# Kernel tuning notes

Measured on AMD Instinct MI355X. Metric: run time of the kernel, lower is better.

## Reference

```python
import jax, jax.numpy as jnp
import numpy as np

B, C, H, W = 64, 2048, 14, 14
D, S, ITERS, EPS, HID = 256, 8, 3, 1e-8, 512


def build_pos(h, w, d):
    gy, gx = np.meshgrid(np.arange(h), np.arange(w), indexing='ij')
    q = d // 4
    omega = 1.0 / (10000.0 ** (np.arange(q) / q))
    ey = gy.reshape(-1, 1) * omega
    ex = gx.reshape(-1, 1) * omega
    pe = np.concatenate([np.sin(ey), np.cos(ey), np.sin(ex), np.cos(ex)], axis=1)
    return jnp.asarray(pe[None], jnp.float32)  # (1, h*w, d)


def layernorm(x, g, b, eps=1e-5):
    m = x.mean(-1, keepdims=True)
    v = ((x - m) ** 2).mean(-1, keepdims=True)
    return (x - m) * jax.lax.rsqrt(v + eps) * g + b


def setup_inputs() -> dict:
    key = jax.random.key(0)
    ks = jax.random.split(key, 16)
    w = lambda k, shp, s=0.02: jax.random.normal(k, shp, jnp.float32) * s
    inp = {
        'x': jax.random.normal(ks[0], (B, C, H, W), jnp.float32),
        'slot_noise': jax.random.normal(ks[1], (B, S, D), jnp.float32),
        'conv_w': w(ks[2], (C, D)), 'conv_b': jnp.zeros((D,), jnp.float32),
        'pos': build_pos(H, W, D),
        'slots_mu': jax.random.normal(ks[3], (1, 1, D), jnp.float32),
        'slots_logsigma': -jnp.ones((1, 1, D), jnp.float32),
        'qw': w(ks[4], (D, D)), 'qb': jnp.zeros((D,), jnp.float32),
        'kw': w(ks[5], (D, D)), 'kb': jnp.zeros((D,), jnp.float32),
        'vw': w(ks[6], (D, D)), 'vb': jnp.zeros((D,), jnp.float32),
        'gru_wih': w(ks[7], (D, 3 * D)), 'gru_whh': w(ks[8], (D, 3 * D)),
        'gru_bih': jnp.zeros((3 * D,), jnp.float32), 'gru_bhh': jnp.zeros((3 * D,), jnp.float32),
        'w1': w(ks[9], (D, HID)), 'b1': jnp.zeros((HID,), jnp.float32),
        'w2': w(ks[10], (HID, D)), 'b2': jnp.zeros((D,), jnp.float32),
        'ln_in_g': jnp.ones((D,), jnp.float32), 'ln_in_b': jnp.zeros((D,), jnp.float32),
        'ln_s_g': jnp.ones((D,), jnp.float32), 'ln_s_b': jnp.zeros((D,), jnp.float32),
        'ln_ff_g': jnp.ones((D,), jnp.float32), 'ln_ff_b': jnp.zeros((D,), jnp.float32),
    }
    return inp


def reference(x, slot_noise, conv_w, conv_b, pos, slots_mu, slots_logsigma,
              qw, qb, kw, kb, vw, vb, gru_wih, gru_whh, gru_bih, gru_bhh,
              w1, b1, w2, b2, ln_in_g, ln_in_b, ln_s_g, ln_s_b, ln_ff_g, ln_ff_b):
    b, c, h, w_ = x.shape
    d = qw.shape[0]
    scale = d ** (-0.5)
    # (B,C,H,W) -> (B,N,C) -> project -> add pos
    xt = x.transpose(0, 2, 3, 1).reshape(b, h * w_, c)
    xt = xt @ conv_w + conv_b + pos
    # slot init
    slots = slots_mu + jnp.exp(slots_logsigma) * slot_noise  # (B,S,D)
    inp = layernorm(xt, ln_in_g, ln_in_b)
    k = inp @ kw + kb
    v = inp @ vw + vb
    attn = None
    for _ in range(ITERS):
        slots_prev = slots
        s = layernorm(slots, ln_s_g, ln_s_b)
        q = s @ qw + qb
        dots = jnp.einsum('bid,bjd->bij', q, k) * scale  # (B,S,N)
        attn = jax.nn.softmax(dots, axis=1) + EPS  # softmax over slots
        attn = attn / attn.sum(-1, keepdims=True)  # renormalize over keys
        updates = jnp.einsum('bjd,bij->bid', v, attn)  # (B,S,D)
        # GRUCell (torch semantics)
        gi = updates @ gru_wih + gru_bih
        gh = slots_prev @ gru_whh + gru_bhh
        ir, iz, inn = jnp.split(gi, 3, axis=-1)
        hr, hz, hn = jnp.split(gh, 3, axis=-1)
        r = jax.nn.sigmoid(ir + hr)
        z = jax.nn.sigmoid(iz + hz)
        nn_ = jnp.tanh(inn + r * hn)
        slots = (1.0 - z) * nn_ + z * slots_prev
        ff = layernorm(slots, ln_ff_g, ln_ff_b)
        slots = slots + (jax.nn.relu(ff @ w1 + b1)) @ w2 + b2
    attn_map = attn.reshape(b, S, h, w_)
    return slots, attn_map
```

## Files before the change

kernel.cpp:

```cpp
#include <hip/hip_runtime.h>
#include <stdint.h>

#define HWN 196
#define CIN 2048
#define DD  256
#define BB  64
#define NSLOT 8
#define PPAD 256
#define KVPAD 224

typedef __attribute__((ext_vector_type(8))) short short8;
typedef __attribute__((ext_vector_type(4))) float f32x4;
typedef __attribute__((ext_vector_type(4))) unsigned short us4;

__device__ __forceinline__ ushort f2bf(float f){ union{float f;uint32_t u;}v;v.f=f;uint32_t u=v.u;return (ushort)((u+0x7FFFu+((u>>16)&1u))>>16);}
__device__ __forceinline__ float bf2f(ushort h){ union{uint32_t u;float f;}v;v.u=((uint32_t)h)<<16;return v.f;}
__device__ __forceinline__ float sigm(float x){ return 1.f/(1.f+expf(-x)); }

__device__ __forceinline__ short8 ldsY(const ushort* buf, int LD, int kt, int lane){
    int row = lane & 15;
    int ch = kt*4 + (lane>>4);
    return *(const short8*)&buf[row*LD + ((ch ^ (row&7))<<3)];
}
__device__ __forceinline__ short8 gX(const ushort* base, int K, int nrow, int kt, int lane){
    return *(const short8*)&base[(size_t)nrow*K + kt*32 + (lane>>4)*8];
}

struct TD { const float* s; ushort* d; int R, C, t0; };
struct TD8 { TD a[8]; };

__global__ __launch_bounds__(256) void k_prep(TD8 td){
    __shared__ float tile[32][33];
    int bt = blockIdx.x;
    int mi = 0;
    #pragma unroll
    for (int i = 1; i < 8; ++i) if (bt >= td.a[i].t0) mi = i;
    TD d = td.a[mi];
    int lt = bt - d.t0;
    int tilesx = (d.C + 31) >> 5;
    int cb = (lt % tilesx) * 32, rb = (lt / tilesx) * 32;
    int tx = threadIdx.x & 31, ty = threadIdx.x >> 5;
    for (int i = ty; i < 32; i += 8) {
        int r = rb + i, c = cb + tx;
        tile[i][tx] = (r < d.R && c < d.C) ? d.s[(size_t)r * d.C + c] : 0.f;
    }
    __syncthreads();
    for (int i = ty; i < 32; i += 8) {
        int c = cb + i, r = rb + tx;
        if (c < d.C && r < d.R) d.d[(size_t)c * d.R + r] = f2bf(tile[tx][i]);
    }
}

__global__ __launch_bounds__(512) void k_proj(const float* __restrict__ x,
        const ushort* __restrict__ bT, const float* __restrict__ cb,
        const float* __restrict__ pos, const float* __restrict__ lng,
        const float* __restrict__ lnb, ushort* __restrict__ inp){
    __shared__ ushort As[2][64*64];
    __shared__ ushort Bs[2][256*64];
    __shared__ float lnpart[64][4][2];
    __shared__ float lnstat[64][2];
    const int t = threadIdx.x, lane = t & 63, wv = t >> 6;
    const int wm = wv >> 2, wn = wv & 3;
    const int b = blockIdx.x >> 2;
    const int p0 = (blockIdx.x & 3) * 64;

    const int am = t & 63, akg = t >> 6;
    const int ap = p0 + am;
    const bool aval = ap < HWN;
    const float* aptr = x + ((size_t)b * CIN) * HWN + ap;

    f32x4 acc[2][4] = {};
    float areg[8];
    short8 breg[4];

    #pragma unroll
    for (int j = 0; j < 8; ++j) areg[j] = aval ? aptr[(size_t)(akg*8+j)*HWN] : 0.f;
    #pragma unroll
    for (int p = 0; p < 4; ++p){
        int idx = p*512 + t; int n = idx>>3, ch = idx&7;
        breg[p] = *(const short8*)&bT[(size_t)n*CIN + ch*8];
    }
    {
        short8 av;
        #pragma unroll
        for (int j = 0; j < 8; ++j) av[j] = (short)f2bf(areg[j]);
        *(short8*)&As[0][am*64 + ((akg^(am&7))<<3)] = av;
        #pragma unroll
        for (int p = 0; p < 4; ++p){
            int idx = p*512 + t; int n = idx>>3, ch = idx&7;
            *(short8*)&Bs[0][n*64 + ((ch^(n&7))<<3)] = breg[p];
        }
    }
    __syncthreads();
    int cur = 0;
    for (int kt = 0; kt < 32; ++kt){
        int k0n = (kt+1)*64;
        if (kt < 31){
            #pragma unroll
            for (int j = 0; j < 8; ++j) areg[j] = aval ? aptr[(size_t)(k0n + akg*8+j)*HWN] : 0.f;
            #pragma unroll
            for (int p = 0; p < 4; ++p){
                int idx = p*512 + t; int n = idx>>3, ch = idx&7;
                breg[p] = *(const short8*)&bT[(size_t)n*CIN + k0n + ch*8];
            }
        }
        #pragma unroll
        for (int kk = 0; kk < 2; ++kk){
            short8 afr[2], bfr[4];
            #pragma unroll
            for (int mi = 0; mi < 2; ++mi){
                int row = wm*32 + mi*16 + (lane&15);
                int ch = kk*4 + (lane>>4);
                afr[mi] = *(const short8*)&As[cur][row*64 + ((ch^(row&7))<<3)];
            }
            #pragma unroll
            for (int ni = 0; ni < 4; ++ni){
                int row = wn*64 + ni*16 + (lane&15);
                int ch = kk*4 + (lane>>4);
                bfr[ni] = *(const short8*)&Bs[cur][row*64 + ((ch^(row&7))<<3)];
            }
            #pragma unroll
            for (int mi = 0; mi < 2; ++mi)
                #pragma unroll
                for (int ni = 0; ni < 4; ++ni)
                    acc[mi][ni] = __builtin_amdgcn_mfma_f32_16x16x32_bf16(afr[mi], bfr[ni], acc[mi][ni], 0,0,0);
        }
        if (kt < 31){
            short8 av;
            #pragma unroll
            for (int j = 0; j < 8; ++j) av[j] = (short)f2bf(areg[j]);
            *(short8*)&As[cur^1][am*64 + ((akg^(am&7))<<3)] = av;
            #pragma unroll
            for (int p = 0; p < 4; ++p){
                int idx = p*512 + t; int n = idx>>3, ch = idx&7;
                *(short8*)&Bs[cur^1][n*64 + ((ch^(n&7))<<3)] = breg[p];
            }
        }
        __syncthreads();
        cur ^= 1;
    }
    #pragma unroll
    for (int mi = 0; mi < 2; ++mi){
        #pragma unroll
        for (int r = 0; r < 4; ++r){
            int row = wm*32 + mi*16 + (lane>>4)*4 + r;
            int p = p0 + row;
            float s = 0.f, ss = 0.f;
            #pragma unroll
            for (int ni = 0; ni < 4; ++ni){
                int n = wn*64 + ni*16 + (lane&15);
                float v = 0.f;
                if (p < HWN) v = acc[mi][ni][r] + cb[n] + pos[(size_t)p*DD + n];
                acc[mi][ni][r] = v;
                s += v; ss += v*v;
            }
            #pragma unroll
            for (int m = 8; m >= 1; m >>= 1){ s += __shfl_xor(s, m, 64); ss += __shfl_xor(ss, m, 64); }
            if ((lane & 15) == 0){ lnpart[row][wn][0] = s; lnpart[row][wn][1] = ss; }
        }
    }
    __syncthreads();
    if (t < 64){
        float lsum = 0.f, lsumsq = 0.f;
        #pragma unroll
        for (int i = 0; i < 4; ++i){ lsum += lnpart[t][i][0]; lsumsq += lnpart[t][i][1]; }
        float mean = lsum * (1.f/256.f);
        float var = lsumsq * (1.f/256.f) - mean*mean;
        lnstat[t][0] = mean; lnstat[t][1] = rsqrtf(var + 1e-5f);
    }
    __syncthreads();
    #pragma unroll
    for (int mi = 0; mi < 2; ++mi){
        #pragma unroll
        for (int ni = 0; ni < 4; ++ni){
            int n = wn*64 + ni*16 + (lane&15);
            float gn = lng[n], bn = lnb[n];
            #pragma unroll
            for (int r = 0; r < 4; ++r){
                int row = wm*32 + mi*16 + (lane>>4)*4 + r;
                float o = (acc[mi][ni][r] - lnstat[row][0]) * lnstat[row][1] * gn + bn;
                inp[((size_t)b*PPAD + p0 + row)*DD + n] = f2bf(o);
            }
        }
    }
}

__global__ __launch_bounds__(512) void k_kv(const ushort* __restrict__ inp,
        const ushort* __restrict__ kwT, const ushort* __restrict__ vwT,
        const float* __restrict__ kb, const float* __restrict__ vb,
        ushort* __restrict__ kbf, ushort* __restrict__ vT){
    __shared__ ushort As[32*256];
    const int t = threadIdx.x, lane = t & 63, wv = t >> 6;
    const int b = blockIdx.x / 7, pblk = blockIdx.x % 7;
    const ushort* arow = inp + ((size_t)b*PPAD + pblk*32)*DD;
    #pragma unroll
    for (int p = 0; p < 2; ++p){
        int idx = p*512 + t; int row = idx>>5, ch = idx&31;
        short8 v = *(const short8*)&arow[(size_t)row*DD + ch*8];
        *(short8*)&As[row*256 + ((ch^(row&7))<<3)] = v;
    }
    __syncthreads();
    f32x4 acck[2][2] = {}, accv[2][2] = {};
    const int n0 = wv*32;
    #pragma unroll
    for (int kt = 0; kt < 8; ++kt){
        short8 afr[2];
        #pragma unroll
        for (int mi = 0; mi < 2; ++mi){
            int row = mi*16 + (lane&15);
            int ch = kt*4 + (lane>>4);
            afr[mi] = *(const short8*)&As[row*256 + ((ch^(row&7))<<3)];
        }
        #pragma unroll
        for (int ni = 0; ni < 2; ++ni){
            int n = n0 + ni*16 + (lane&15);
            int koff = kt*32 + (lane>>4)*8;
            short8 bk = *(const short8*)&kwT[(size_t)n*DD + koff];
            short8 bv = *(const short8*)&vwT[(size_t)n*DD + koff];
            #pragma unroll
            for (int mi = 0; mi < 2; ++mi){
                acck[mi][ni] = __builtin_amdgcn_mfma_f32_16x16x32_bf16(afr[mi], bk, acck[mi][ni],0,0,0);
                accv[mi][ni] = __builtin_amdgcn_mfma_f32_16x16x32_bf16(afr[mi], bv, accv[mi][ni],0,0,0);
            }
        }
    }
    #pragma unroll
    for (int mi = 0; mi < 2; ++mi){
        #pragma unroll
        for (int ni = 0; ni < 2; ++ni){
            int n = n0 + ni*16 + (lane&15);
            float kbn = kb[n], vbn = vb[n];
            int pl0 = pblk*32 + mi*16 + (lane>>4)*4;
            us4 pk;
            #pragma unroll
            for (int r = 0; r < 4; ++r){
                kbf[((size_t)b*KVPAD + pl0 + r)*DD + n] = f2bf(acck[mi][ni][r] + kbn);
                pk[r] = f2bf(accv[mi][ni][r] + vbn);
            }
            *(us4*)&vT[((size_t)b*DD + n)*KVPAD + pl0] = pk;
        }
    }
}

__global__ __launch_bounds__(512) void k_init(const float* __restrict__ noise,
        const float* __restrict__ mu, const float* __restrict__ lsig,
        const ushort* __restrict__ qwT, const float* __restrict__ qb,
        const float* __restrict__ gs, const float* __restrict__ bs,
        float* __restrict__ slots, ushort* __restrict__ qbuf){
    __shared__ float Sld[16*256];
    __shared__ ushort Ysn[16*256];
    __shared__ float part[8][16][2];
    __shared__ float stats[16][2];
    const int t = threadIdx.x, lane = t & 63, w = t >> 6;
    const int bb = blockIdx.x, rbase = bb*16;
    {
        int row = t>>5, ch = t&31; int d = ch*8;
        f32x4 n0 = *(const f32x4*)&noise[(size_t)(rbase+row)*DD + d];
        f32x4 n1 = *(const f32x4*)&noise[(size_t)(rbase+row)*DD + d + 4];
        f32x4 m0 = *(const f32x4*)&mu[d];
        f32x4 m1 = *(const f32x4*)&mu[d+4];
        f32x4 l0 = *(const f32x4*)&lsig[d];
        f32x4 l1 = *(const f32x4*)&lsig[d+4];
        f32x4 s0, s1;
        #pragma unroll
        for (int j = 0; j < 4; ++j){
            s0[j] = m0[j] + expf(l0[j])*n0[j];
            s1[j] = m1[j] + expf(l1[j])*n1[j];
        }
        *(f32x4*)&slots[(size_t)(rbase+row)*DD + d] = s0;
        *(f32x4*)&slots[(size_t)(rbase+row)*DD + d + 4] = s1;
        *(f32x4*)&Sld[row*256 + d] = s0;
        *(f32x4*)&Sld[row*256 + d + 4] = s1;
    }
    __syncthreads();
    f32x4 sv[2];
    #pragma unroll
    for (int sub = 0; sub < 2; ++sub){
        int d0 = w*32 + sub*16 + (lane>>4)*4;
        sv[sub] = *(const f32x4*)&Sld[(lane&15)*256 + d0];
    }
    {
        float lsum = 0.f, lsq = 0.f;
        #pragma unroll
        for (int sub = 0; sub < 2; ++sub)
            #pragma unroll
            for (int r = 0; r < 4; ++r){ float v = sv[sub][r]; lsum += v; lsq += v*v; }
        lsum += __shfl_xor(lsum, 16, 64); lsum += __shfl_xor(lsum, 32, 64);
        lsq  += __shfl_xor(lsq, 16, 64);  lsq  += __shfl_xor(lsq, 32, 64);
        if (lane < 16){ part[w][lane][0] = lsum; part[w][lane][1] = lsq; }
    }
    __syncthreads();
    if (t < 16){
        float a = 0.f, c = 0.f;
        #pragma unroll
        for (int i = 0; i < 8; ++i){ a += part[i][t][0]; c += part[i][t][1]; }
        float mean = a*(1.f/256.f);
        stats[t][0] = mean;
        stats[t][1] = rsqrtf(c*(1.f/256.f) - mean*mean + 1e-5f);
    }
    __syncthreads();
    {
        int slot = lane&15;
        float mean = stats[slot][0], rs = stats[slot][1];
        #pragma unroll
        for (int sub = 0; sub < 2; ++sub){
            int d0 = w*32 + sub*16 + (lane>>4)*4;
            f32x4 g4 = *(const f32x4*)&gs[d0];
            f32x4 b4 = *(const f32x4*)&bs[d0];
            us4 o;
            #pragma unroll
            for (int r = 0; r < 4; ++r) o[r] = f2bf((sv[sub][r]-mean)*rs*g4[r] + b4[r]);
            int ch = d0>>3;
            *(us4*)&Ysn[slot*256 + ((ch^(slot&7))<<3) + (d0&7)] = o;
        }
    }
    __syncthreads();
    f32x4 qa[2] = {};
    #pragma unroll
    for (int kt = 0; kt < 8; ++kt){
        short8 ysn = ldsY(Ysn, 256, kt, lane);
        #pragma unroll
        for (int sub = 0; sub < 2; ++sub){
            int nrow = w*32 + sub*16 + (lane&15);
            short8 x = gX(qwT, 256, nrow, kt, lane);
            qa[sub] = __builtin_amdgcn_mfma_f32_16x16x32_bf16(x, ysn, qa[sub], 0,0,0);
        }
    }
    #pragma unroll
    for (int sub = 0; sub < 2; ++sub){
        int qd0 = w*32 + sub*16 + (lane>>4)*4;
        f32x4 qb4 = *(const f32x4*)&qb[qd0];
        us4 o;
        #pragma unroll
        for (int r = 0; r < 4; ++r) o[r] = f2bf((qa[sub][r]+qb4[r])*0.0625f);
        *(us4*)&qbuf[(size_t)(rbase+(lane&15))*DD + qd0] = o;
    }
}

__global__ __launch_bounds__(256) void k_attn(const ushort* __restrict__ qbuf,
        const ushort* __restrict__ kbf, const ushort* __restrict__ vT,
        ushort* __restrict__ upd, float* __restrict__ out_attn, int writeAttn){
    __shared__ ushort Yq[16*256];
    __shared__ ushort Xat[16*256];
    __shared__ float wpart[4][16];
    __shared__ float invk[16];
    const int t = threadIdx.x, lane = t & 63, w = t >> 6;
    const int b = blockIdx.x;
    {
        int row = t>>5, ch = t&31;
        short8 v = *(const short8*)&qbuf[(size_t)(b*NSLOT+row)*DD + ch*8];
        *(short8*)&Yq[row*256 + ((ch^(row&7))<<3)] = v;
        int row2 = row + 8;
        short8 z;
        #pragma unroll
        for (int j = 0; j < 8; ++j) z[j] = 0;
        *(short8*)&Yq[row2*256 + ((ch^(row2&7))<<3)] = z;
    }
    __syncthreads();
    short8 yf[8];
    #pragma unroll
    for (int kt = 0; kt < 8; ++kt) yf[kt] = ldsY(Yq, 256, kt, lane);
    float ps = 0.f;
    const int nf = (w < 3) ? 4 : 2;
    for (int i = 0; i < nf; ++i){
        int f = w*4 + i;
        f32x4 acc = {};
        #pragma unroll
        for (int kt = 0; kt < 8; ++kt){
            short8 x = gX(kbf + (size_t)b*KVPAD*DD, 256, f*16 + (lane&15), kt, lane);
            acc = __builtin_amdgcn_mfma_f32_16x16x32_bf16(x, yf[kt], acc, 0,0,0);
        }
        int k0 = f*16 + (lane>>4)*4;
        us4 o;
        #pragma unroll
        for (int r = 0; r < 4; ++r){
            float v = acc[r];
            float mx = v;
            mx = fmaxf(mx, __shfl_xor(mx, 1, 64));
            mx = fmaxf(mx, __shfl_xor(mx, 2, 64));
            mx = fmaxf(mx, __shfl_xor(mx, 4, 64));
            float e = expf(v - mx);
            float se = e;
            se += __shfl_xor(se, 1, 64);
            se += __shfl_xor(se, 2, 64);
            se += __shfl_xor(se, 4, 64);
            float val = e/se + 1e-8f;
            if (k0 + r >= HWN) val = 0.f;
            ps += val;
            o[r] = f2bf(val);
        }
        int slot = lane & 15;
        int ch = k0 >> 3;
        *(us4*)&Xat[slot*256 + ((ch^(slot&7))<<3) + (k0&7)] = o;
    }
    ps += __shfl_xor(ps, 16, 64);
    ps += __shfl_xor(ps, 32, 64);
    if (lane < 16) wpart[w][lane] = ps;
    __syncthreads();
    if (t < 16) invk[t] = 1.f/(wpart[0][t] + wpart[1][t] + wpart[2][t] + wpart[3][t]);
    __syncthreads();
    short8 xa[7];
    #pragma unroll
    for (int kt = 0; kt < 7; ++kt) xa[kt] = ldsY(Xat, 256, kt, lane);
    #pragma unroll
    for (int i = 0; i < 4; ++i){
        int d0 = (w*4 + i)*16;
        f32x4 acc = {};
        #pragma unroll
        for (int kt = 0; kt < 7; ++kt){
            short8 y = gX(vT + (size_t)b*DD*KVPAD, KVPAD, d0 + (lane&15), kt, lane);
            acc = __builtin_amdgcn_mfma_f32_16x16x32_bf16(xa[kt], y, acc, 0,0,0);
        }
        #pragma unroll
        for (int r = 0; r < 4; ++r){
            int slot = (lane>>4)*4 + r;
            if (slot < NSLOT)
                upd[(size_t)(b*NSLOT+slot)*DD + d0 + (lane&15)] = f2bf(acc[r]*invk[slot]);
        }
    }
    if (writeAttn){
        for (int idx = t; idx < NSLOT*HWN; idx += 256){
            int slot = idx/HWN, key = idx - slot*HWN;
            int ch = key >> 3;
            float v = bf2f(Xat[slot*256 + ((ch^(slot&7))<<3) + (key&7)]);
            out_attn[(size_t)b*NSLOT*HWN + idx] = v*invk[slot];
        }
    }
}

__global__ __launch_bounds__(512) void k_upd(
        const ushort* __restrict__ upd, float* __restrict__ slots,
        ushort* __restrict__ qbuf,
        const ushort* __restrict__ wihT, const ushort* __restrict__ whhT,
        const float* __restrict__ bih, const float* __restrict__ bhh,
        const ushort* __restrict__ w1T, const float* __restrict__ b1,
        const ushort* __restrict__ w2T, const float* __restrict__ b2,
        const float* __restrict__ gff, const float* __restrict__ bff,
        const float* __restrict__ gs, const float* __restrict__ bs,
        const ushort* __restrict__ qwT, const float* __restrict__ qb,
        float* __restrict__ out_slots, int final_){
    __shared__ ushort Yupd[16*256];
    __shared__ ushort Yslb[16*256];
    __shared__ ushort Ysn[16*256];
    __shared__ ushort Yh[16*512];
    __shared__ float part[8][16][2];
    __shared__ float stats[16][2];
    const int t = threadIdx.x, lane = t & 63, w = t >> 6;
    const int bb = blockIdx.x, rbase = bb*16;
    {
        int row = t>>5, ch = t&31;
        short8 uv = *(const short8*)&upd[(size_t)(rbase+row)*DD + ch*8];
        *(short8*)&Yupd[row*256 + ((ch^(row&7))<<3)] = uv;
        f32x4 s0 = *(const f32x4*)&slots[(size_t)(rbase+row)*DD + ch*8];
        f32x4 s1 = *(const f32x4*)&slots[(size_t)(rbase+row)*DD + ch*8 + 4];
        short8 sv;
        #pragma unroll
        for (int j = 0; j < 4; ++j){ sv[j] = (short)f2bf(s0[j]); sv[4+j] = (short)f2bf(s1[j]); }
        *(short8*)&Yslb[row*256 + ((ch^(row&7))<<3)] = sv;
    }
    __syncthreads();
    f32x4 gi[6] = {}, gh[6] = {};
    #pragma unroll
    for (int kt = 0; kt < 8; ++kt){
        short8 yu = ldsY(Yupd, 256, kt, lane);
        short8 ys = ldsY(Yslb, 256, kt, lane);
        #pragma unroll
        for (int g = 0; g < 3; ++g)
            #pragma unroll
            for (int sub = 0; sub < 2; ++sub){
                int nrow = g*256 + w*32 + sub*16 + (lane&15);
                short8 xi = gX(wihT, 256, nrow, kt, lane);
                short8 xh = gX(whhT, 256, nrow, kt, lane);
                gi[g*2+sub] = __builtin_amdgcn_mfma_f32_16x16x32_bf16(xi, yu, gi[g*2+sub], 0,0,0);
                gh[g*2+sub] = __builtin_amdgcn_mfma_f32_16x16x32_bf16(xh, ys, gh[g*2+sub], 0,0,0);
            }
    }
    f32x4 snew[2];
    #pragma unroll
    for (int sub = 0; sub < 2; ++sub){
        int d0 = w*32 + sub*16 + (lane>>4)*4;
        f32x4 sp  = *(const f32x4*)&slots[(size_t)(rbase + (lane&15))*DD + d0];
        f32x4 bir = *(const f32x4*)&bih[d0];
        f32x4 biz = *(const f32x4*)&bih[256 + d0];
        f32x4 bin = *(const f32x4*)&bih[512 + d0];
        f32x4 bhr = *(const f32x4*)&bhh[d0];
        f32x4 bhz = *(const f32x4*)&bhh[256 + d0];
        f32x4 bhn = *(const f32x4*)&bhh[512 + d0];
        #pragma unroll
        for (int r = 0; r < 4; ++r){
            float ir = gi[0+sub][r] + bir[r];
            float iz = gi[2+sub][r] + biz[r];
            float in_ = gi[4+sub][r] + bin[r];
            float hr = gh[0+sub][r] + bhr[r];
            float hz = gh[2+sub][r] + bhz[r];
            float hn = gh[4+sub][r] + bhn[r];
            float rr = sigm(ir + hr);
            float zz = sigm(iz + hz);
            float nn = tanhf(in_ + rr*hn);
            snew[sub][r] = (1.f - zz)*nn + zz*sp[r];
        }
    }
    {
        float lsum = 0.f, lsq = 0.f;
        #pragma unroll
        for (int sub = 0; sub < 2; ++sub)
            #pragma unroll
            for (int r = 0; r < 4; ++r){ float v = snew[sub][r]; lsum += v; lsq += v*v; }
        lsum += __shfl_xor(lsum, 16, 64); lsum += __shfl_xor(lsum, 32, 64);
        lsq  += __shfl_xor(lsq, 16, 64);  lsq  += __shfl_xor(lsq, 32, 64);
        if (lane < 16){ part[w][lane][0] = lsum; part[w][lane][1] = lsq; }
    }
    __syncthreads();
    if (t < 16){
        float a = 0.f, c = 0.f;
        #pragma unroll
        for (int i = 0; i < 8; ++i){ a += part[i][t][0]; c += part[i][t][1]; }
        float mean = a*(1.f/256.f);
        stats[t][0] = mean;
        stats[t][1] = rsqrtf(c*(1.f/256.f) - mean*mean + 1e-5f);
    }
    __syncthreads();
    {
        int slot = lane & 15;
        float mean = stats[slot][0], rs = stats[slot][1];
        #pragma unroll
        for (int sub = 0; sub < 2; ++sub){
            int d0 = w*32 + sub*16 + (lane>>4)*4;
            f32x4 g4 = *(const f32x4*)&gff[d0];
            f32x4 b4 = *(const f32x4*)&bff[d0];
            us4 o;
            #pragma unroll
            for (int r = 0; r < 4; ++r) o[r] = f2bf((snew[sub][r]-mean)*rs*g4[r] + b4[r]);
            int ch = d0 >> 3;
            *(us4*)&Ysn[slot*256 + ((ch^(slot&7))<<3) + (d0&7)] = o;
        }
    }
    __syncthreads();
    f32x4 hh[4] = {};
    #pragma unroll
    for (int kt = 0; kt < 8; ++kt){
        short8 ysn = ldsY(Ysn, 256, kt, lane);
        #pragma unroll
        for (int s2 = 0; s2 < 4; ++s2){
            int nrow = w*64 + s2*16 + (lane&15);
            short8 x = gX(w1T, 256, nrow, kt, lane);
            hh[s2] = __builtin_amdgcn_mfma_f32_16x16x32_bf16(x, ysn, hh[s2], 0,0,0);
        }
    }
    {
        int row = lane & 15;
        #pragma unroll
        for (int s2 = 0; s2 < 4; ++s2){
            int n0 = w*64 + s2*16 + (lane>>4)*4;
            f32x4 b14 = *(const f32x4*)&b1[n0];
            us4 o;
            #pragma unroll
            for (int r = 0; r < 4; ++r) o[r] = f2bf(fmaxf(hh[s2][r] + b14[r], 0.f));
            int ch = n0 >> 3;
            *(us4*)&Yh[row*512 + ((ch^(row&7))<<3) + (n0&7)] = o;
        }
    }
    __syncthreads();
    f32x4 o2[2] = {};
    #pragma unroll
    for (int kt = 0; kt < 16; ++kt){
        short8 yh = ldsY(Yh, 512, kt, lane);
        #pragma unroll
        for (int sub = 0; sub < 2; ++sub){
            int nrow = w*32 + sub*16 + (lane&15);
            short8 x = gX(w2T, 512, nrow, kt, lane);
            o2[sub] = __builtin_amdgcn_mfma_f32_16x16x32_bf16(x, yh, o2[sub], 0,0,0);
        }
    }
    f32x4 ns[2];
    {
        float* dst = final_ ? out_slots : slots;
        #pragma unroll
        for (int sub = 0; sub < 2; ++sub){
            int d0 = w*32 + sub*16 + (lane>>4)*4;
            f32x4 b24 = *(const f32x4*)&b2[d0];
            #pragma unroll
            for (int r = 0; r < 4; ++r) ns[sub][r] = o2[sub][r] + b24[r] + snew[sub][r];
            *(f32x4*)&dst[(size_t)(rbase + (lane&15))*DD + d0] = ns[sub];
        }
    }
    if (final_) return;
    {
        float lsum = 0.f, lsq = 0.f;
        #pragma unroll
        for (int sub = 0; sub < 2; ++sub)
            #pragma unroll
            for (int r = 0; r < 4; ++r){ float v = ns[sub][r]; lsum += v; lsq += v*v; }
        lsum += __shfl_xor(lsum, 16, 64); lsum += __shfl_xor(lsum, 32, 64);
        lsq  += __shfl_xor(lsq, 16, 64);  lsq  += __shfl_xor(lsq, 32, 64);
        if (lane < 16){ part[w][lane][0] = lsum; part[w][lane][1] = lsq; }
    }
    __syncthreads();
    if (t < 16){
        float a = 0.f, c = 0.f;
        #pragma unroll
        for (int i = 0; i < 8; ++i){ a += part[i][t][0]; c += part[i][t][1]; }
        float mean = a*(1.f/256.f);
        stats[t][0] = mean;
        stats[t][1] = rsqrtf(c*(1.f/256.f) - mean*mean + 1e-5f);
    }
    __syncthreads();
    {
        int slot = lane & 15;
        float mean = stats[slot][0], rs = stats[slot][1];
        #pragma unroll
        for (int sub = 0; sub < 2; ++sub){
            int d0 = w*32 + sub*16 + (lane>>4)*4;
            f32x4 g4 = *(const f32x4*)&gs[d0];
            f32x4 b4 = *(const f32x4*)&bs[d0];
            us4 o;
            #pragma unroll
            for (int r = 0; r < 4; ++r) o[r] = f2bf((ns[sub][r]-mean)*rs*g4[r] + b4[r]);
            int ch = d0 >> 3;
            *(us4*)&Ysn[slot*256 + ((ch^(slot&7))<<3) + (d0&7)] = o;
        }
    }
    __syncthreads();
    f32x4 qa[2] = {};
    #pragma unroll
    for (int kt = 0; kt < 8; ++kt){
        short8 ysn = ldsY(Ysn, 256, kt, lane);
        #pragma unroll
        for (int sub = 0; sub < 2; ++sub){
            int nrow = w*32 + sub*16 + (lane&15);
            short8 x = gX(qwT, 256, nrow, kt, lane);
            qa[sub] = __builtin_amdgcn_mfma_f32_16x16x32_bf16(x, ysn, qa[sub], 0,0,0);
        }
    }
    #pragma unroll
    for (int sub = 0; sub < 2; ++sub){
        int qd0 = w*32 + sub*16 + (lane>>4)*4;
        f32x4 qb4 = *(const f32x4*)&qb[qd0];
        us4 o;
        #pragma unroll
        for (int r = 0; r < 4; ++r) o[r] = f2bf((qa[sub][r]+qb4[r])*0.0625f);
        *(us4*)&qbuf[(size_t)(rbase+(lane&15))*DD + qd0] = o;
    }
}

extern "C" void kernel_launch(void* const* d_in, const int* in_sizes, int n_in,
                              void* d_out, int out_size, void* d_ws, size_t ws_size,
                              hipStream_t stream) {
    const float* x      = (const float*)d_in[0];
    const float* noise  = (const float*)d_in[1];
    const float* conv_w = (const float*)d_in[2];
    const float* conv_b = (const float*)d_in[3];
    const float* pos    = (const float*)d_in[4];
    const float* mu     = (const float*)d_in[5];
    const float* logsig = (const float*)d_in[6];
    const float* qw  = (const float*)d_in[7];
    const float* qb  = (const float*)d_in[8];
    const float* kw  = (const float*)d_in[9];
    const float* kb  = (const float*)d_in[10];
    const float* vw  = (const float*)d_in[11];
    const float* vb  = (const float*)d_in[12];
    const float* wih = (const float*)d_in[13];
    const float* whh = (const float*)d_in[14];
    const float* bih = (const float*)d_in[15];
    const float* bhh = (const float*)d_in[16];
    const float* w1  = (const float*)d_in[17];
    const float* b1  = (const float*)d_in[18];
    const float* w2  = (const float*)d_in[19];
    const float* b2  = (const float*)d_in[20];
    const float* g_in = (const float*)d_in[21];
    const float* b_in = (const float*)d_in[22];
    const float* g_s  = (const float*)d_in[23];
    const float* b_s  = (const float*)d_in[24];
    const float* g_ff = (const float*)d_in[25];
    const float* b_ff = (const float*)d_in[26];

    char* w = (char*)d_ws;
    ushort* inp_bf = (ushort*)w; w += (size_t)BB*PPAD*DD*2;
    ushort* kbf    = (ushort*)w; w += (size_t)BB*KVPAD*DD*2;
    ushort* vT     = (ushort*)w; w += (size_t)BB*DD*KVPAD*2;
    ushort* cwT    = (ushort*)w; w += (size_t)DD*CIN*2;
    ushort* qwT    = (ushort*)w; w += (size_t)DD*DD*2;
    ushort* kwT    = (ushort*)w; w += (size_t)DD*DD*2;
    ushort* vwT    = (ushort*)w; w += (size_t)DD*DD*2;
    ushort* wihT   = (ushort*)w; w += (size_t)768*DD*2;
    ushort* whhT   = (ushort*)w; w += (size_t)768*DD*2;
    ushort* w1T    = (ushort*)w; w += (size_t)512*DD*2;
    ushort* w2T    = (ushort*)w; w += (size_t)DD*512*2;
    ushort* qbb    = (ushort*)w; w += (size_t)BB*NSLOT*DD*2;
    ushort* updb   = (ushort*)w; w += (size_t)BB*NSLOT*DD*2;
    float*  slotsb = (float*)w;  w += (size_t)BB*NSLOT*DD*4;

    float* out_slots = (float*)d_out;
    float* out_attn  = (float*)d_out + (size_t)BB*NSLOT*DD;

    TD8 td;
    td.a[0] = { conv_w, cwT, 2048, 256,    0 };
    td.a[1] = { qw,     qwT,  256, 256,  512 };
    td.a[2] = { kw,     kwT,  256, 256,  576 };
    td.a[3] = { vw,     vwT,  256, 256,  640 };
    td.a[4] = { wih,    wihT, 256, 768,  704 };
    td.a[5] = { whh,    whhT, 256, 768,  896 };
    td.a[6] = { w1,     w1T,  256, 512, 1088 };
    td.a[7] = { w2,     w2T,  512, 256, 1216 };

    k_prep<<<1344, 256, 0, stream>>>(td);
    k_proj<<<256, 512, 0, stream>>>(x, cwT, conv_b, pos, g_in, b_in, inp_bf);
    k_kv<<<448, 512, 0, stream>>>(inp_bf, kwT, vwT, kb, vb, kbf, vT);
    k_init<<<32, 512, 0, stream>>>(noise, mu, logsig, qwT, qb, g_s, b_s, slotsb, qbb);
    for (int it = 0; it < 3; ++it){
        k_attn<<<64, 256, 0, stream>>>(qbb, kbf, vT, updb, out_attn, it == 2);
        k_upd<<<32, 512, 0, stream>>>(updb, slotsb, qbb, wihT, whhT, bih, bhh,
                                      w1T, b1, w2T, b2, g_ff, b_ff, g_s, b_s,
                                      qwT, qb, out_slots, it == 2);
    }
}
```

Baseline: 259.7 us.

## Retile projection GEMM over flat rows, move input LN into k_kv, fuse attn+update

The conv projection GEMM now tiles over the flattened B*HW rows with 64x128 tiles on a 2x196 grid, so padded rows are no longer computed and more blocks are launched. The input layernorm moves out of the GEMM epilogue and into the k_kv prologue, reading bf16 rows and normalizing them before the K/V projection. The per-iteration attention and GRU/MLP update kernels are merged into one k_slot kernel per batch, which drops a launch and the updates round-trip through global memory. In exchange, the fused kernel runs 8 valid slots inside 16-row MFMA tiles, and the layernorm now works on bf16-rounded values.

```diff
diff --git a/kernel.cpp b/kernel.cpp
--- a/kernel.cpp
+++ b/kernel.cpp
@@ -6,8 +6,8 @@
 #define DD  256
 #define BB  64
 #define NSLOT 8
-#define PPAD 256
 #define KVPAD 224
+#define MTOT 12544
 
 typedef __attribute__((ext_vector_type(8))) short short8;
 typedef __attribute__((ext_vector_type(4))) float f32x4;
@@ -53,42 +53,40 @@
 
 __global__ __launch_bounds__(512) void k_proj(const float* __restrict__ x,
         const ushort* __restrict__ bT, const float* __restrict__ cb,
-        const float* __restrict__ pos, const float* __restrict__ lng,
-        const float* __restrict__ lnb, ushort* __restrict__ inp){
+        const float* __restrict__ pos, ushort* __restrict__ xt){
     __shared__ ushort As[2][64*64];
-    __shared__ ushort Bs[2][256*64];
-    __shared__ float lnpart[64][4][2];
-    __shared__ float lnstat[64][2];
+    __shared__ ushort Bs[2][128*64];
     const int t = threadIdx.x, lane = t & 63, wv = t >> 6;
     const int wm = wv >> 2, wn = wv & 3;
-    const int b = blockIdx.x >> 2;
-    const int p0 = (blockIdx.x & 3) * 64;
+    const int bm = blockIdx.y * 64;
+    const int bn = blockIdx.x * 128;
 
     const int am = t & 63, akg = t >> 6;
-    const int ap = p0 + am;
-    const bool aval = ap < HWN;
-    const float* aptr = x + ((size_t)b * CIN) * HWN + ap;
-
-    f32x4 acc[2][4] = {};
+    const int mg = bm + am;
+    const int ab = mg / HWN, ap = mg % HWN;
+    const float* aptr = x + (size_t)ab * (CIN * HWN) + ap;
+
+    const int bnl = t >> 2;
+    const int bch0 = (t & 3) * 2;
+    const ushort* bptr = bT + (size_t)(bn + bnl) * CIN;
+
+    f32x4 acc[2][2] = {};
     float areg[8];
-    short8 breg[4];
-
-    #pragma unroll
-    for (int j = 0; j < 8; ++j) areg[j] = aval ? aptr[(size_t)(akg*8+j)*HWN] : 0.f;
-    #pragma unroll
-    for (int p = 0; p < 4; ++p){
-        int idx = p*512 + t; int n = idx>>3, ch = idx&7;
-        breg[p] = *(const short8*)&bT[(size_t)n*CIN + ch*8];
-    }
+    short8 breg[2];
+
+    #pragma unroll
+    for (int j = 0; j < 8; ++j) areg[j] = aptr[(size_t)(akg*8+j)*HWN];
+    #pragma unroll
+    for (int c = 0; c < 2; ++c) breg[c] = *(const short8*)&bptr[(bch0+c)*8];
     {
         short8 av;
         #pragma unroll
         for (int j = 0; j < 8; ++j) av[j] = (short)f2bf(areg[j]);
         *(short8*)&As[0][am*64 + ((akg^(am&7))<<3)] = av;
         #pragma unroll
-        for (int p = 0; p < 4; ++p){
-            int idx = p*512 + t; int n = idx>>3, ch = idx&7;
-            *(short8*)&Bs[0][n*64 + ((ch^(n&7))<<3)] = breg[p];
+        for (int c = 0; c < 2; ++c){
+            int ch = bch0 + c;
+            *(short8*)&Bs[0][bnl*64 + ((ch^(bnl&7))<<3)] = breg[c];
         }
     }
     __syncthreads();
@@ -97,16 +95,13 @@
         int k0n = (kt+1)*64;
         if (kt < 31){
             #pragma unroll
-            for (int j = 0; j < 8; ++j) areg[j] = aval ? aptr[(size_t)(k0n + akg*8+j)*HWN] : 0.f;
-            #pragma unroll
-            for (int p = 0; p < 4; ++p){
-                int idx = p*512 + t; int n = idx>>3, ch = idx&7;
-                breg[p] = *(const short8*)&bT[(size_t)n*CIN + k0n + ch*8];
-            }
+            for (int j = 0; j < 8; ++j) areg[j] = aptr[(size_t)(k0n + akg*8+j)*HWN];
+            #pragma unroll
+            for (int c = 0; c < 2; ++c) breg[c] = *(const short8*)&bptr[k0n + (bch0+c)*8];
         }
         #pragma unroll
         for (int kk = 0; kk < 2; ++kk){
-            short8 afr[2], bfr[4];
+            short8 afr[2], bfr[2];
             #pragma unroll
             for (int mi = 0; mi < 2; ++mi){
                 int row = wm*32 + mi*16 + (lane&15);
@@ -114,15 +109,15 @@
                 afr[mi] = *(const short8*)&As[cur][row*64 + ((ch^(row&7))<<3)];
             }
             #pragma unroll
-            for (int ni = 0; ni < 4; ++ni){
-                int row = wn*64 + ni*16 + (lane&15);
+            for (int ni = 0; ni < 2; ++ni){
+                int row = wn*32 + ni*16 + (lane&15);
                 int ch = kk*4 + (lane>>4);
                 bfr[ni] = *(const short8*)&Bs[cur][row*64 + ((ch^(row&7))<<3)];
             }
             #pragma unroll
             for (int mi = 0; mi < 2; ++mi)
                 #pragma unroll
-                for (int ni = 0; ni < 4; ++ni)
+                for (int ni = 0; ni < 2; ++ni)
                     acc[mi][ni] = __builtin_amdgcn_mfma_f32_16x16x32_bf16(afr[mi], bfr[ni], acc[mi][ni], 0,0,0);
         }
         if (kt < 31){
@@ -131,9 +126,9 @@
             for (int j = 0; j < 8; ++j) av[j] = (short)f2bf(areg[j]);
             *(short8*)&As[cur^1][am*64 + ((akg^(am&7))<<3)] = av;
             #pragma unroll
-            for (int p = 0; p < 4; ++p){
-                int idx = p*512 + t; int n = idx>>3, ch = idx&7;
-                *(short8*)&Bs[cur^1][n*64 + ((ch^(n&7))<<3)] = breg[p];
+            for (int c = 0; c < 2; ++c){
+                int ch = bch0 + c;
+                *(short8*)&Bs[cur^1][bnl*64 + ((ch^(bnl&7))<<3)] = breg[c];
             }
         }
         __syncthreads();
@@ -142,62 +137,55 @@
     #pragma unroll
     for (int mi = 0; mi < 2; ++mi){
         #pragma unroll
-        for (int r = 0; r < 4; ++r){
-            int row = wm*32 + mi*16 + (lane>>4)*4 + r;
-            int p = p0 + row;
-            float s = 0.f, ss = 0.f;
-            #pragma unroll
-            for (int ni = 0; ni < 4; ++ni){
-                int n = wn*64 + ni*16 + (lane&15);
-                float v = 0.f;
-                if (p < HWN) v = acc[mi][ni][r] + cb[n] + pos[(size_t)p*DD + n];
-                acc[mi][ni][r] = v;
-                s += v; ss += v*v;
-            }
-            #pragma unroll
-            for (int m = 8; m >= 1; m >>= 1){ s += __shfl_xor(s, m, 64); ss += __shfl_xor(ss, m, 64); }
-            if ((lane & 15) == 0){ lnpart[row][wn][0] = s; lnpart[row][wn][1] = ss; }
-        }
-    }
-    __syncthreads();
-    if (t < 64){
-        float lsum = 0.f, lsumsq = 0.f;
-        #pragma unroll
-        for (int i = 0; i < 4; ++i){ lsum += lnpart[t][i][0]; lsumsq += lnpart[t][i][1]; }
-        float mean = lsum * (1.f/256.f);
-        float var = lsumsq * (1.f/256.f) - mean*mean;
-        lnstat[t][0] = mean; lnstat[t][1] = rsqrtf(var + 1e-5f);
-    }
-    __syncthreads();
-    #pragma unroll
-    for (int mi = 0; mi < 2; ++mi){
-        #pragma unroll
-        for (int ni = 0; ni < 4; ++ni){
-            int n = wn*64 + ni*16 + (lane&15);
-            float gn = lng[n], bn = lnb[n];
+        for (int ni = 0; ni < 2; ++ni){
+            int n = bn + wn*32 + ni*16 + (lane&15);
+            float cbn = cb[n];
             #pragma unroll
             for (int r = 0; r < 4; ++r){
                 int row = wm*32 + mi*16 + (lane>>4)*4 + r;
-                float o = (acc[mi][ni][r] - lnstat[row][0]) * lnstat[row][1] * gn + bn;
-                inp[((size_t)b*PPAD + p0 + row)*DD + n] = f2bf(o);
+                int m = bm + row;
+                int p = m % HWN;
+                xt[(size_t)m*DD + n] = f2bf(acc[mi][ni][r] + cbn + pos[(size_t)p*DD + n]);
             }
         }
     }
 }
 
-__global__ __launch_bounds__(512) void k_kv(const ushort* __restrict__ inp,
+__global__ __launch_bounds__(512) void k_kv(const ushort* __restrict__ xt,
         const ushort* __restrict__ kwT, const ushort* __restrict__ vwT,
         const float* __restrict__ kb, const float* __restrict__ vb,
+        const float* __restrict__ lng, const float* __restrict__ lnb,
         ushort* __restrict__ kbf, ushort* __restrict__ vT){
     __shared__ ushort As[32*256];
     const int t = threadIdx.x, lane = t & 63, wv = t >> 6;
     const int b = blockIdx.x / 7, pblk = blockIdx.x % 7;
-    const ushort* arow = inp + ((size_t)b*PPAD + pblk*32)*DD;
-    #pragma unroll
-    for (int p = 0; p < 2; ++p){
-        int idx = p*512 + t; int row = idx>>5, ch = idx&31;
-        short8 v = *(const short8*)&arow[(size_t)row*DD + ch*8];
-        *(short8*)&As[row*256 + ((ch^(row&7))<<3)] = v;
+    {
+        int row = t >> 4, seg = t & 15;
+        int grow = b*HWN + pblk*32 + row;
+        if (grow > MTOT-1) grow = MTOT-1;
+        const ushort* src = &xt[(size_t)grow*DD + seg*16];
+        short8 v0 = *(const short8*)&src[0];
+        short8 v1 = *(const short8*)&src[8];
+        float f[16];
+        #pragma unroll
+        for (int j = 0; j < 8; ++j){ f[j] = bf2f((ushort)v0[j]); f[8+j] = bf2f((ushort)v1[j]); }
+        float s = 0.f, sq = 0.f;
+        #pragma unroll
+        for (int j = 0; j < 16; ++j){ s += f[j]; sq += f[j]*f[j]; }
+        #pragma unroll
+        for (int m = 8; m >= 1; m >>= 1){ s += __shfl_xor(s, m, 64); sq += __shfl_xor(sq, m, 64); }
+        float mean = s * (1.f/256.f);
+        float rs = rsqrtf(sq*(1.f/256.f) - mean*mean + 1e-5f);
+        int d0 = seg*16;
+        short8 o0, o1;
+        #pragma unroll
+        for (int j = 0; j < 8; ++j){
+            o0[j] = (short)f2bf((f[j]   - mean)*rs*lng[d0+j]   + lnb[d0+j]);
+            o1[j] = (short)f2bf((f[8+j] - mean)*rs*lng[d0+8+j] + lnb[d0+8+j]);
+        }
+        int ch0 = seg*2;
+        *(short8*)&As[row*256 + ((ch0^(row&7))<<3)] = o0;
+        *(short8*)&As[row*256 + (((ch0+1)^(row&7))<<3)] = o1;
     }
     __syncthreads();
     f32x4 acck[2][2] = {}, accv[2][2] = {};
@@ -322,8 +310,8 @@
         #pragma unroll
         for (int sub = 0; sub < 2; ++sub){
             int nrow = w*32 + sub*16 + (lane&15);
-            short8 x = gX(qwT, 256, nrow, kt, lane);
-            qa[sub] = __builtin_amdgcn_mfma_f32_16x16x32_bf16(x, ysn, qa[sub], 0,0,0);
+            short8 xx = gX(qwT, 256, nrow, kt, lane);
+            qa[sub] = __builtin_amdgcn_mfma_f32_16x16x32_bf16(xx, ysn, qa[sub], 0,0,0);
         }
     }
     #pragma unroll
@@ -337,100 +325,10 @@
     }
 }
 
-__global__ __launch_bounds__(256) void k_attn(const ushort* __restrict__ qbuf,
-        const ushort* __restrict__ kbf, const ushort* __restrict__ vT,
-        ushort* __restrict__ upd, float* __restrict__ out_attn, int writeAttn){
-    __shared__ ushort Yq[16*256];
-    __shared__ ushort Xat[16*256];
-    __shared__ float wpart[4][16];
-    __shared__ float invk[16];
-    const int t = threadIdx.x, lane = t & 63, w = t >> 6;
-    const int b = blockIdx.x;
-    {
-        int row = t>>5, ch = t&31;
-        short8 v = *(const short8*)&qbuf[(size_t)(b*NSLOT+row)*DD + ch*8];
-        *(short8*)&Yq[row*256 + ((ch^(row&7))<<3)] = v;
-        int row2 = row + 8;
-        short8 z;
-        #pragma unroll
-        for (int j = 0; j < 8; ++j) z[j] = 0;
-        *(short8*)&Yq[row2*256 + ((ch^(row2&7))<<3)] = z;
-    }
-    __syncthreads();
-    short8 yf[8];
-    #pragma unroll
-    for (int kt = 0; kt < 8; ++kt) yf[kt] = ldsY(Yq, 256, kt, lane);
-    float ps = 0.f;
-    const int nf = (w < 3) ? 4 : 2;
-    for (int i = 0; i < nf; ++i){
-        int f = w*4 + i;
-        f32x4 acc = {};
-        #pragma unroll
-        for (int kt = 0; kt < 8; ++kt){
-            short8 x = gX(kbf + (size_t)b*KVPAD*DD, 256, f*16 + (lane&15), kt, lane);
-            acc = __builtin_amdgcn_mfma_f32_16x16x32_bf16(x, yf[kt], acc, 0,0,0);
-        }
-        int k0 = f*16 + (lane>>4)*4;
-        us4 o;
-        #pragma unroll
-        for (int r = 0; r < 4; ++r){
-            float v = acc[r];
-            float mx = v;
-            mx = fmaxf(mx, __shfl_xor(mx, 1, 64));
-            mx = fmaxf(mx, __shfl_xor(mx, 2, 64));
-            mx = fmaxf(mx, __shfl_xor(mx, 4, 64));
-            float e = expf(v - mx);
-            float se = e;
-            se += __shfl_xor(se, 1, 64);
-            se += __shfl_xor(se, 2, 64);
-            se += __shfl_xor(se, 4, 64);
-            float val = e/se + 1e-8f;
-            if (k0 + r >= HWN) val = 0.f;
-            ps += val;
-            o[r] = f2bf(val);
-        }
-        int slot = lane & 15;
-        int ch = k0 >> 3;
-        *(us4*)&Xat[slot*256 + ((ch^(slot&7))<<3) + (k0&7)] = o;
-    }
-    ps += __shfl_xor(ps, 16, 64);
-    ps += __shfl_xor(ps, 32, 64);
-    if (lane < 16) wpart[w][lane] = ps;
-    __syncthreads();
-    if (t < 16) invk[t] = 1.f/(wpart[0][t] + wpart[1][t] + wpart[2][t] + wpart[3][t]);
-    __syncthreads();
-    short8 xa[7];
-    #pragma unroll
-    for (int kt = 0; kt < 7; ++kt) xa[kt] = ldsY(Xat, 256, kt, lane);
-    #pragma unroll
-    for (int i = 0; i < 4; ++i){
-        int d0 = (w*4 + i)*16;
-        f32x4 acc = {};
-        #pragma unroll
-        for (int kt = 0; kt < 7; ++kt){
-            short8 y = gX(vT + (size_t)b*DD*KVPAD, KVPAD, d0 + (lane&15), kt, lane);
-            acc = __builtin_amdgcn_mfma_f32_16x16x32_bf16(xa[kt], y, acc, 0,0,0);
-        }
-        #pragma unroll
-        for (int r = 0; r < 4; ++r){
-            int slot = (lane>>4)*4 + r;
-            if (slot < NSLOT)
-                upd[(size_t)(b*NSLOT+slot)*DD + d0 + (lane&15)] = f2bf(acc[r]*invk[slot]);
-        }
-    }
-    if (writeAttn){
-        for (int idx = t; idx < NSLOT*HWN; idx += 256){
-            int slot = idx/HWN, key = idx - slot*HWN;
-            int ch = key >> 3;
-            float v = bf2f(Xat[slot*256 + ((ch^(slot&7))<<3) + (key&7)]);
-            out_attn[(size_t)b*NSLOT*HWN + idx] = v*invk[slot];
-        }
-    }
-}
-
-__global__ __launch_bounds__(512) void k_upd(
-        const ushort* __restrict__ upd, float* __restrict__ slots,
-        ushort* __restrict__ qbuf,
+__global__ __launch_bounds__(512) void k_slot(
+        const ushort* __restrict__ qbuf, const ushort* __restrict__ kbf,
+        const ushort* __restrict__ vT, float* __restrict__ slots,
+        ushort* __restrict__ qout,
         const ushort* __restrict__ wihT, const ushort* __restrict__ whhT,
         const float* __restrict__ bih, const float* __restrict__ bhh,
         const ushort* __restrict__ w1T, const float* __restrict__ b1,
@@ -438,25 +336,127 @@
         const float* __restrict__ gff, const float* __restrict__ bff,
         const float* __restrict__ gs, const float* __restrict__ bs,
         const ushort* __restrict__ qwT, const float* __restrict__ qb,
-        float* __restrict__ out_slots, int final_){
+        float* __restrict__ out_slots, float* __restrict__ out_attn,
+        int final_){
+    __shared__ ushort Yq[16*256];
+    __shared__ ushort Xat[16*256];
     __shared__ ushort Yupd[16*256];
     __shared__ ushort Yslb[16*256];
     __shared__ ushort Ysn[16*256];
     __shared__ ushort Yh[16*512];
+    __shared__ float wpart[8][16];
+    __shared__ float invk[16];
     __shared__ float part[8][16][2];
     __shared__ float stats[16][2];
     const int t = threadIdx.x, lane = t & 63, w = t >> 6;
-    const int bb = blockIdx.x, rbase = bb*16;
-    {
+    const int b = blockIdx.x;
+    const int rbase = b * NSLOT;
+    const int srow = lane & 15;
+    const int srd = (srow < NSLOT) ? srow : 0;
+
+    if (t < 256){
         int row = t>>5, ch = t&31;
-        short8 uv = *(const short8*)&upd[(size_t)(rbase+row)*DD + ch*8];
-        *(short8*)&Yupd[row*256 + ((ch^(row&7))<<3)] = uv;
+        short8 v = *(const short8*)&qbuf[(size_t)(rbase+row)*DD + ch*8];
+        *(short8*)&Yq[row*256 + ((ch^(row&7))<<3)] = v;
         f32x4 s0 = *(const f32x4*)&slots[(size_t)(rbase+row)*DD + ch*8];
         f32x4 s1 = *(const f32x4*)&slots[(size_t)(rbase+row)*DD + ch*8 + 4];
         short8 sv;
         #pragma unroll
         for (int j = 0; j < 4; ++j){ sv[j] = (short)f2bf(s0[j]); sv[4+j] = (short)f2bf(s1[j]); }
         *(short8*)&Yslb[row*256 + ((ch^(row&7))<<3)] = sv;
+    } else {
+        int i = t - 256;
+        int row = (i>>5) + 8, ch = i&31;
+        short8 z;
+        #pragma unroll
+        for (int j = 0; j < 8; ++j) z[j] = 0;
+        *(short8*)&Yq[row*256 + ((ch^(row&7))<<3)] = z;
+        *(short8*)&Yupd[row*256 + ((ch^(row&7))<<3)] = z;
+        *(short8*)&Yslb[row*256 + ((ch^(row&7))<<3)] = z;
+    }
+    __syncthreads();
+    {
+        short8 yf[8];
+        #pragma unroll
+        for (int kt = 0; kt < 8; ++kt) yf[kt] = ldsY(Yq, 256, kt, lane);
+        float ps = 0.f;
+        #pragma unroll
+        for (int rep = 0; rep < 2; ++rep){
+            int f = w + rep*8;
+            if (f < 14){
+                f32x4 acc = {};
+                #pragma unroll
+                for (int kt = 0; kt < 8; ++kt){
+                    short8 xx = gX(kbf + (size_t)b*KVPAD*DD, 256, f*16 + (lane&15), kt, lane);
+                    acc = __builtin_amdgcn_mfma_f32_16x16x32_bf16(xx, yf[kt], acc, 0,0,0);
+                }
+                int k0 = f*16 + (lane>>4)*4;
+                us4 o;
+                #pragma unroll
+                for (int r = 0; r < 4; ++r){
+                    float v = acc[r];
+                    float mx = v;
+                    mx = fmaxf(mx, __shfl_xor(mx, 1, 64));
+                    mx = fmaxf(mx, __shfl_xor(mx, 2, 64));
+                    mx = fmaxf(mx, __shfl_xor(mx, 4, 64));
+                    float e = expf(v - mx);
+                    float se = e;
+                    se += __shfl_xor(se, 1, 64);
+                    se += __shfl_xor(se, 2, 64);
+                    se += __shfl_xor(se, 4, 64);
+                    float val = e/se + 1e-8f;
+                    if (k0 + r >= HWN) val = 0.f;
+                    ps += val;
+                    o[r] = f2bf(val);
+                }
+                int ch = k0 >> 3;
+                *(us4*)&Xat[srow*256 + ((ch^(srow&7))<<3) + (k0&7)] = o;
+            }
+        }
+        ps += __shfl_xor(ps, 16, 64);
+        ps += __shfl_xor(ps, 32, 64);
+        if (lane < 16) wpart[w][lane] = ps;
+    }
+    __syncthreads();
+    if (t < 16){
+        float s = 0.f;
+        #pragma unroll
+        for (int i = 0; i < 8; ++i) s += wpart[i][t];
+        invk[t] = 1.f/s;
+    }
+    __syncthreads();
+    {
+        short8 xa[7];
+        #pragma unroll
+        for (int kt = 0; kt < 7; ++kt) xa[kt] = ldsY(Xat, 256, kt, lane);
+        f32x4 iv = *(const f32x4*)&invk[(lane>>4)*4];
+        #pragma unroll
+        for (int i = 0; i < 2; ++i){
+            int d0 = (w*2 + i)*16;
+            f32x4 acc = {};
+            #pragma unroll
+            for (int kt = 0; kt < 7; ++kt){
+                short8 y = gX(vT + (size_t)b*DD*KVPAD, KVPAD, d0 + (lane&15), kt, lane);
+                acc = __builtin_amdgcn_mfma_f32_16x16x32_bf16(xa[kt], y, acc, 0,0,0);
+            }
+            #pragma unroll
+            for (int r = 0; r < 4; ++r){
+                int s2 = (lane>>4)*4 + r;
+                if (s2 < NSLOT){
+                    int d = d0 + (lane&15);
+                    int ch = d >> 3;
+                    Yupd[s2*256 + ((ch^(s2&7))<<3) + (d&7)] = f2bf(acc[r]*iv[r]);
+                }
+            }
+        }
+    }
+    if (final_){
+        for (int idx = t; idx < NSLOT*HWN; idx += 512){
+            int slot = idx/HWN, key = idx - slot*HWN;
+            int ch = key >> 3;
+            out_attn[(size_t)b*NSLOT*HWN + idx] =
+                bf2f(Xat[slot*256 + ((ch^(slot&7))<<3) + (key&7)]) * invk[slot];
+        }
     }
     __syncthreads();
     f32x4 gi[6] = {}, gh[6] = {};
@@ -479,7 +479,7 @@
     #pragma unroll
     for (int sub = 0; sub < 2; ++sub){
         int d0 = w*32 + sub*16 + (lane>>4)*4;
-        f32x4 sp  = *(const f32x4*)&slots[(size_t)(rbase + (lane&15))*DD + d0];
+        f32x4 sp  = *(const f32x4*)&slots[(size_t)(rbase + srd)*DD + d0];
         f32x4 bir = *(const f32x4*)&bih[d0];
         f32x4 biz = *(const f32x4*)&bih[256 + d0];
         f32x4 bin = *(const f32x4*)&bih[512 + d0];
@@ -521,8 +521,7 @@
     }
     __syncthreads();
     {
-        int slot = lane & 15;
-        float mean = stats[slot][0], rs = stats[slot][1];
+        float mean = stats[srow][0], rs = stats[srow][1];
         #pragma unroll
         for (int sub = 0; sub < 2; ++sub){
             int d0 = w*32 + sub*16 + (lane>>4)*4;
@@ -532,23 +531,22 @@
             #pragma unroll
             for (int r = 0; r < 4; ++r) o[r] = f2bf((snew[sub][r]-mean)*rs*g4[r] + b4[r]);
             int ch = d0 >> 3;
-            *(us4*)&Ysn[slot*256 + ((ch^(slot&7))<<3) + (d0&7)] = o;
-        }
-    }
-    __syncthreads();
-    f32x4 hh[4] = {};
-    #pragma unroll
-    for (int kt = 0; kt < 8; ++kt){
-        short8 ysn = ldsY(Ysn, 256, kt, lane);
-        #pragma unroll
-        for (int s2 = 0; s2 < 4; ++s2){
-            int nrow = w*64 + s2*16 + (lane&15);
-            short8 x = gX(w1T, 256, nrow, kt, lane);
-            hh[s2] = __builtin_amdgcn_mfma_f32_16x16x32_bf16(x, ysn, hh[s2], 0,0,0);
-        }
-    }
-    {
-        int row = lane & 15;
+            *(us4*)&Ysn[srow*256 + ((ch^(srow&7))<<3) + (d0&7)] = o;
+        }
+    }
+    __syncthreads();
+    {
+        f32x4 hh[4] = {};
+        #pragma unroll
+        for (int kt = 0; kt < 8; ++kt){
+            short8 ysn = ldsY(Ysn, 256, kt, lane);
+            #pragma unroll
+            for (int s2 = 0; s2 < 4; ++s2){
+                int nrow = w*64 + s2*16 + (lane&15);
+                short8 xx = gX(w1T, 256, nrow, kt, lane);
+                hh[s2] = __builtin_amdgcn_mfma_f32_16x16x32_bf16(xx, ysn, hh[s2], 0,0,0);
+            }
+        }
         #pragma unroll
         for (int s2 = 0; s2 < 4; ++s2){
             int n0 = w*64 + s2*16 + (lane>>4)*4;
@@ -557,23 +555,23 @@
             #pragma unroll
             for (int r = 0; r < 4; ++r) o[r] = f2bf(fmaxf(hh[s2][r] + b14[r], 0.f));
             int ch = n0 >> 3;
-            *(us4*)&Yh[row*512 + ((ch^(row&7))<<3) + (n0&7)] = o;
-        }
-    }
-    __syncthreads();
-    f32x4 o2[2] = {};
-    #pragma unroll
-    for (int kt = 0; kt < 16; ++kt){
-        short8 yh = ldsY(Yh, 512, kt, lane);
-        #pragma unroll
-        for (int sub = 0; sub < 2; ++sub){
-            int nrow = w*32 + sub*16 + (lane&15);
-            short8 x = gX(w2T, 512, nrow, kt, lane);
-            o2[sub] = __builtin_amdgcn_mfma_f32_16x16x32_bf16(x, yh, o2[sub], 0,0,0);
-        }
-    }
+            *(us4*)&Yh[srow*512 + ((ch^(srow&7))<<3) + (n0&7)] = o;
+        }
+    }
+    __syncthreads();
     f32x4 ns[2];
     {
+        f32x4 o2[2] = {};
+        #pragma unroll
+        for (int kt = 0; kt < 16; ++kt){
+            short8 yh = ldsY(Yh, 512, kt, lane);
+            #pragma unroll
+            for (int sub = 0; sub < 2; ++sub){
+                int nrow = w*32 + sub*16 + (lane&15);
+                short8 xx = gX(w2T, 512, nrow, kt, lane);
+                o2[sub] = __builtin_amdgcn_mfma_f32_16x16x32_bf16(xx, yh, o2[sub], 0,0,0);
+            }
+        }
         float* dst = final_ ? out_slots : slots;
         #pragma unroll
         for (int sub = 0; sub < 2; ++sub){
@@ -581,7 +579,8 @@
             f32x4 b24 = *(const f32x4*)&b2[d0];
             #pragma unroll
             for (int r = 0; r < 4; ++r) ns[sub][r] = o2[sub][r] + b24[r] + snew[sub][r];
-            *(f32x4*)&dst[(size_t)(rbase + (lane&15))*DD + d0] = ns[sub];
+            if (srow < NSLOT)
+                *(f32x4*)&dst[(size_t)(rbase + srow)*DD + d0] = ns[sub];
         }
     }
     if (final_) return;
@@ -606,8 +605,7 @@
     }
     __syncthreads();
     {
-        int slot = lane & 15;
-        float mean = stats[slot][0], rs = stats[slot][1];
+        float mean = stats[srow][0], rs = stats[srow][1];
         #pragma unroll
         for (int sub = 0; sub < 2; ++sub){
             int d0 = w*32 + sub*16 + (lane>>4)*4;
@@ -617,29 +615,32 @@
             #pragma unroll
             for (int r = 0; r < 4; ++r) o[r] = f2bf((ns[sub][r]-mean)*rs*g4[r] + b4[r]);
             int ch = d0 >> 3;
-            *(us4*)&Ysn[slot*256 + ((ch^(slot&7))<<3) + (d0&7)] = o;
-        }
-    }
-    __syncthreads();
-    f32x4 qa[2] = {};
-    #pragma unroll
-    for (int kt = 0; kt < 8; ++kt){
-        short8 ysn = ldsY(Ysn, 256, kt, lane);
+            *(us4*)&Ysn[srow*256 + ((ch^(srow&7))<<3) + (d0&7)] = o;
+        }
+    }
+    __syncthreads();
+    {
+        f32x4 qa[2] = {};
+        #pragma unroll
+        for (int kt = 0; kt < 8; ++kt){
+            short8 ysn = ldsY(Ysn, 256, kt, lane);
+            #pragma unroll
+            for (int sub = 0; sub < 2; ++sub){
+                int nrow = w*32 + sub*16 + (lane&15);
+                short8 xx = gX(qwT, 256, nrow, kt, lane);
+                qa[sub] = __builtin_amdgcn_mfma_f32_16x16x32_bf16(xx, ysn, qa[sub], 0,0,0);
+            }
+        }
         #pragma unroll
         for (int sub = 0; sub < 2; ++sub){
-            int nrow = w*32 + sub*16 + (lane&15);
-            short8 x = gX(qwT, 256, nrow, kt, lane);
-            qa[sub] = __builtin_amdgcn_mfma_f32_16x16x32_bf16(x, ysn, qa[sub], 0,0,0);
-        }
-    }
-    #pragma unroll
-    for (int sub = 0; sub < 2; ++sub){
-        int qd0 = w*32 + sub*16 + (lane>>4)*4;
-        f32x4 qb4 = *(const f32x4*)&qb[qd0];
-        us4 o;
-        #pragma unroll
-        for (int r = 0; r < 4; ++r) o[r] = f2bf((qa[sub][r]+qb4[r])*0.0625f);
-        *(us4*)&qbuf[(size_t)(rbase+(lane&15))*DD + qd0] = o;
+            int qd0 = w*32 + sub*16 + (lane>>4)*4;
+            f32x4 qb4 = *(const f32x4*)&qb[qd0];
+            us4 o;
+            #pragma unroll
+            for (int r = 0; r < 4; ++r) o[r] = f2bf((qa[sub][r]+qb4[r])*0.0625f);
+            if (srow < NSLOT)
+                *(us4*)&qout[(size_t)(rbase + srow)*DD + qd0] = o;
+        }
     }
 }
 
@@ -675,7 +676,7 @@
     const float* b_ff = (const float*)d_in[26];
 
     char* w = (char*)d_ws;
-    ushort* inp_bf = (ushort*)w; w += (size_t)BB*PPAD*DD*2;
+    ushort* xt     = (ushort*)w; w += (size_t)MTOT*DD*2;
     ushort* kbf    = (ushort*)w; w += (size_t)BB*KVPAD*DD*2;
     ushort* vT     = (ushort*)w; w += (size_t)BB*DD*KVPAD*2;
     ushort* cwT    = (ushort*)w; w += (size_t)DD*CIN*2;
@@ -687,7 +688,6 @@
     ushort* w1T    = (ushort*)w; w += (size_t)512*DD*2;
     ushort* w2T    = (ushort*)w; w += (size_t)DD*512*2;
     ushort* qbb    = (ushort*)w; w += (size_t)BB*NSLOT*DD*2;
-    ushort* updb   = (ushort*)w; w += (size_t)BB*NSLOT*DD*2;
     float*  slotsb = (float*)w;  w += (size_t)BB*NSLOT*DD*4;
 
     float* out_slots = (float*)d_out;
@@ -704,13 +704,13 @@
     td.a[7] = { w2,     w2T,  512, 256, 1216 };
 
     k_prep<<<1344, 256, 0, stream>>>(td);
-    k_proj<<<256, 512, 0, stream>>>(x, cwT, conv_b, pos, g_in, b_in, inp_bf);
-    k_kv<<<448, 512, 0, stream>>>(inp_bf, kwT, vwT, kb, vb, kbf, vT);
+    k_proj<<<dim3(2, 196), 512, 0, stream>>>(x, cwT, conv_b, pos, xt);
+    k_kv<<<448, 512, 0, stream>>>(xt, kwT, vwT, kb, vb, g_in, b_in, kbf, vT);
     k_init<<<32, 512, 0, stream>>>(noise, mu, logsig, qwT, qb, g_s, b_s, slotsb, qbb);
     for (int it = 0; it < 3; ++it){
-        k_attn<<<64, 256, 0, stream>>>(qbb, kbf, vT, updb, out_attn, it == 2);
-        k_upd<<<32, 512, 0, stream>>>(updb, slotsb, qbb, wihT, whhT, bih, bhh,
-                                      w1T, b1, w2T, b2, g_ff, b_ff, g_s, b_s,
-                                      qwT, qb, out_slots, it == 2);
+        k_slot<<<BB, 512, 0, stream>>>(qbb, kbf, vT, slotsb, qbb,
+                                       wihT, whhT, bih, bhh, w1T, b1, w2T, b2,
+                                       g_ff, b_ff, g_s, b_s, qwT, qb,
+                                       out_slots, out_attn, it == 2);
     }
 }
```

Result: faster. 243.1 us (-6.4%).
